# Optimization experiments

Measured on AMD Instinct MI355X. Metric: run time of the kernel, lower is better.

## Reference

```python
import jax, jax.numpy as jnp
import numpy as np

B, N, NB, NORB = 8, 128, 32, 128  # batch, particles, single-body basis size, orbitals


def _offdiag_idx(n):
    # [N, N-1] indices of j != i, matching remove_diag with an aux (feature) axis
    return np.stack([np.concatenate([np.arange(i), np.arange(i + 1, n)]) for i in range(n)])


def setup_inputs() -> dict:
    key = jax.random.key(0)
    k1, k2 = jax.random.split(key)
    chi = jax.random.normal(k1, (B, N, NB), dtype=jnp.float32)
    # param('backflow_coeff', normal(stddev=0.01), (Nb*Nb, n_orbitals))
    backflow_coeff = 0.01 * jax.random.normal(k2, (NB * NB, NORB), dtype=jnp.float32)
    return {"chi": chi, "backflow_coeff": backflow_coeff}


def reference(chi, backflow_coeff):
    b, n, nb = chi.shape
    # basis_combine_backflow: chi_munu_ij[b,i,j, k*Nb + l] = chi[b,j,k] * chi[b,i,l]
    # (meshgrid(a=chi_i, b=chi_j) with indexing='xy' -> prod[k,l] = chi_i[l]*chi_j[k], raveled)
    pair = jnp.einsum('bjk,bil->bijkl', chi, chi).reshape(b, n, n, nb * nb)
    # remove_diag(..., has_aux_axis=True): drop j == i along axis 2 -> [B, N, N-1, Nb^2]
    idx = jnp.asarray(_offdiag_idx(n))
    pair = pair[:, jnp.arange(n)[:, None], idx, :]
    # mean over neighbors j != i -> [B, N, Nb^2]
    basis = pair.mean(axis=-2)
    # BF = basis @ backflow_coeff -> [B, N, n_orbitals]
    return basis @ backflow_coeff
```

## Files before the change

### kernel.cpp

```cpp
#include <hip/hip_runtime.h>
#include <hip/hip_bf16.h>

#define B_    8
#define N_    128
#define NB_   32
#define NORB_ 128
#define RPB   32
#define OPB   16
#define THREADS 256

using bf16x8 = __attribute__((ext_vector_type(8))) short;
using f32x4  = __attribute__((ext_vector_type(4))) float;

__global__ __launch_bounds__(THREADS) void bobf_kernel(
    const float* __restrict__ chi,
    const float* __restrict__ W,
    float* __restrict__ out)
{
    __shared__ float wt[1024][18];
    __shared__ float Sp[8][NB_];
    __shared__ float S[NB_];
    __shared__ __align__(16) float xr_[RPB][36];
    __shared__ float yr_[RPB][36];
    __shared__ float red2[4][RPB][20];

    const int t   = threadIdx.x;
    const int blk = blockIdx.x;
    const int b    = blk >> 5;
    const int rowg = (blk >> 3) & 3;
    const int og   = blk & 7;
    const int i0   = rowg * RPB;
    const int o0   = og * OPB;

    #pragma unroll
    for (int e = 0; e < 32; ++e) {
        const int c  = e * THREADS + t;
        const int kl = c >> 3, cc = c & 7;
        const float2 v = *(const float2*)(W + kl * NORB_ + o0 + cc * 2);
        *(float2*)&wt[kl][cc * 2] = v;
    }

    {
        const int k = t & 31;
        const int g = t >> 5;
        const float* base = chi + (b * N_) * NB_ + k;
        float s = 0.f;
        #pragma unroll
        for (int jj = 0; jj < 16; ++jj) s += base[(g * 16 + jj) * NB_];
        Sp[g][k] = s;
    }
    #pragma unroll
    for (int e = 0; e < 4; ++e) {
        const int idx = e * THREADS + t;
        const int r = idx >> 5, l = idx & 31;
        xr_[r][l] = chi[(b * N_ + i0 + r) * NB_ + l];
    }
    __syncthreads();
    if (t < NB_) {
        float s = 0.f;
        #pragma unroll
        for (int g = 0; g < 8; ++g) s += Sp[g][t];
        S[t] = s;
    }
    __syncthreads();
    {
        const float inv = 1.0f / (float)(N_ - 1);
        #pragma unroll
        for (int e = 0; e < 4; ++e) {
            const int idx = e * THREADS + t;
            const int r = idx >> 5, q = idx & 31;
            yr_[r][q] = (S[q] - xr_[r][q]) * inv;
        }
    }
    __syncthreads();

    const int wv   = t >> 6;
    const int lane = t & 63;
    const int lr = lane & 15;
    const int lg = lane >> 4;
    const int l0 = lg * 8;

    float xa0[8], xa1[8];
    #pragma unroll
    for (int e = 0; e < 8; ++e) {
        xa0[e] = xr_[lr][l0 + e];
        xa1[e] = xr_[16 + lr][l0 + e];
    }

    f32x4 acc0 = {0.f, 0.f, 0.f, 0.f};
    f32x4 acc1 = {0.f, 0.f, 0.f, 0.f};

    #pragma unroll
    for (int ks = 0; ks < 8; ++ks) {
        const int kstep = wv * 8 + ks;
        bf16x8 bf;
        #pragma unroll
        for (int e = 0; e < 8; ++e) {
            const float w0 = wt[kstep * 32 + l0 + e][lr];
            bf[e] = (short)__bfloat16_as_ushort(__float2bfloat16(w0));
        }
        const float y0 = yr_[lr][kstep];
        const float y1 = yr_[16 + lr][kstep];
        bf16x8 af0, af1;
        #pragma unroll
        for (int e = 0; e < 8; ++e) {
            af0[e] = (short)__bfloat16_as_ushort(__float2bfloat16(y0 * xa0[e]));
            af1[e] = (short)__bfloat16_as_ushort(__float2bfloat16(y1 * xa1[e]));
        }
        acc0 = __builtin_amdgcn_mfma_f32_16x16x32_bf16(af0, bf, acc0, 0, 0, 0);
        acc1 = __builtin_amdgcn_mfma_f32_16x16x32_bf16(af1, bf, acc1, 0, 0, 0);
    }

    #pragma unroll
    for (int reg = 0; reg < 4; ++reg) {
        red2[wv][lg * 4 + reg][lr]      = acc0[reg];
        red2[wv][16 + lg * 4 + reg][lr] = acc1[reg];
    }
    __syncthreads();
    #pragma unroll
    for (int e = 0; e < 2; ++e) {
        const int idx = e * THREADS + t;
        const int r = idx >> 4, o = idx & 15;
        const float v = red2[0][r][o] + red2[1][r][o] + red2[2][r][o] + red2[3][r][o];
        out[(b * N_ + i0 + r) * NORB_ + o0 + o] = v;
    }
}

extern "C" void kernel_launch(void* const* d_in, const int* in_sizes, int n_in,
                              void* d_out, int out_size, void* d_ws, size_t ws_size,
                              hipStream_t stream) {
    const float* chi = (const float*)d_in[0];
    const float* W   = (const float*)d_in[1];
    float* out = (float*)d_out;
    dim3 grid(B_ * (N_ / RPB) * (NORB_ / OPB));
    dim3 block(THREADS);
    hipLaunchKernelGGL(bobf_kernel, grid, block, 0, stream, chi, W, out);
}
```

Baseline: 9.854 us.

## Load W fragments directly into registers and double threads per block

Removes the LDS staging of the weight tile. Each lane now loads its bf16 B-fragment values straight from global memory into registers, issued before the chi reductions so the loads overlap that work. The block grows to 512 threads (8 waves), each wave taking 4 k-steps instead of 8. The final cross-wave reduction now sums 8 partials. The direct global loads are strided (one column per lane), which trades coalescing for skipping the LDS round trip and one sync's worth of staging.

```diff
diff --git a/kernel.cpp b/kernel.cpp
--- a/kernel.cpp
+++ b/kernel.cpp
@@ -7,7 +7,7 @@
 #define NORB_ 128
 #define RPB   32
 #define OPB   16
-#define THREADS 256
+#define THREADS 512
 
 using bf16x8 = __attribute__((ext_vector_type(8))) short;
 using f32x4  = __attribute__((ext_vector_type(4))) float;
@@ -17,12 +17,11 @@
     const float* __restrict__ W,
     float* __restrict__ out)
 {
-    __shared__ float wt[1024][18];
-    __shared__ float Sp[8][NB_];
+    __shared__ float Sp[16][NB_];
     __shared__ float S[NB_];
     __shared__ __align__(16) float xr_[RPB][36];
     __shared__ float yr_[RPB][36];
-    __shared__ float red2[4][RPB][20];
+    __shared__ float red2[8][RPB][20];
 
     const int t   = threadIdx.x;
     const int blk = blockIdx.x;
@@ -32,12 +31,20 @@
     const int i0   = rowg * RPB;
     const int o0   = og * OPB;
 
+    const int wv   = t >> 6;
+    const int lane = t & 63;
+    const int lr = lane & 15;
+    const int lg = lane >> 4;
+    const int l0 = lg * 8;
+
+    float wf[4][8];
     #pragma unroll
-    for (int e = 0; e < 32; ++e) {
-        const int c  = e * THREADS + t;
-        const int kl = c >> 3, cc = c & 7;
-        const float2 v = *(const float2*)(W + kl * NORB_ + o0 + cc * 2);
-        *(float2*)&wt[kl][cc * 2] = v;
+    for (int ks = 0; ks < 4; ++ks) {
+        const int kstep = wv * 4 + ks;
+        const float* wp = W + (kstep * 32 + l0) * NORB_ + o0 + lr;
+        #pragma unroll
+        for (int e = 0; e < 8; ++e)
+            wf[ks][e] = wp[e * NORB_];
     }
 
     {
@@ -46,11 +53,11 @@
         const float* base = chi + (b * N_) * NB_ + k;
         float s = 0.f;
         #pragma unroll
-        for (int jj = 0; jj < 16; ++jj) s += base[(g * 16 + jj) * NB_];
+        for (int jj = 0; jj < 8; ++jj) s += base[(g * 8 + jj) * NB_];
         Sp[g][k] = s;
     }
     #pragma unroll
-    for (int e = 0; e < 4; ++e) {
+    for (int e = 0; e < 2; ++e) {
         const int idx = e * THREADS + t;
         const int r = idx >> 5, l = idx & 31;
         xr_[r][l] = chi[(b * N_ + i0 + r) * NB_ + l];
@@ -59,14 +66,14 @@
     if (t < NB_) {
         float s = 0.f;
         #pragma unroll
-        for (int g = 0; g < 8; ++g) s += Sp[g][t];
+        for (int g = 0; g < 16; ++g) s += Sp[g][t];
         S[t] = s;
     }
     __syncthreads();
     {
         const float inv = 1.0f / (float)(N_ - 1);
         #pragma unroll
-        for (int e = 0; e < 4; ++e) {
+        for (int e = 0; e < 2; ++e) {
             const int idx = e * THREADS + t;
             const int r = idx >> 5, q = idx & 31;
             yr_[r][q] = (S[q] - xr_[r][q]) * inv;
@@ -74,11 +81,12 @@
     }
     __syncthreads();
 
-    const int wv   = t >> 6;
-    const int lane = t & 63;
-    const int lr = lane & 15;
-    const int lg = lane >> 4;
-    const int l0 = lg * 8;
+    bf16x8 bfr[4];
+    #pragma unroll
+    for (int ks = 0; ks < 4; ++ks)
+        #pragma unroll
+        for (int e = 0; e < 8; ++e)
+            bfr[ks][e] = (short)__bfloat16_as_ushort(__float2bfloat16(wf[ks][e]));
 
     float xa0[8], xa1[8];
     #pragma unroll
@@ -87,28 +95,25 @@
         xa1[e] = xr_[16 + lr][l0 + e];
     }
 
+    bf16x8 af0[4], af1[4];
+    #pragma unroll
+    for (int ks = 0; ks < 4; ++ks) {
+        const int kstep = wv * 4 + ks;
+        const float y0 = yr_[lr][kstep];
+        const float y1 = yr_[16 + lr][kstep];
+        #pragma unroll
+        for (int e = 0; e < 8; ++e) {
+            af0[ks][e] = (short)__bfloat16_as_ushort(__float2bfloat16(y0 * xa0[e]));
+            af1[ks][e] = (short)__bfloat16_as_ushort(__float2bfloat16(y1 * xa1[e]));
+        }
+    }
+
     f32x4 acc0 = {0.f, 0.f, 0.f, 0.f};
     f32x4 acc1 = {0.f, 0.f, 0.f, 0.f};
-
     #pragma unroll
-    for (int ks = 0; ks < 8; ++ks) {
-        const int kstep = wv * 8 + ks;
-        bf16x8 bf;
-        #pragma unroll
-        for (int e = 0; e < 8; ++e) {
-            const float w0 = wt[kstep * 32 + l0 + e][lr];
-            bf[e] = (short)__bfloat16_as_ushort(__float2bfloat16(w0));
-        }
-        const float y0 = yr_[lr][kstep];
-        const float y1 = yr_[16 + lr][kstep];
-        bf16x8 af0, af1;
-        #pragma unroll
-        for (int e = 0; e < 8; ++e) {
-            af0[e] = (short)__bfloat16_as_ushort(__float2bfloat16(y0 * xa0[e]));
-            af1[e] = (short)__bfloat16_as_ushort(__float2bfloat16(y1 * xa1[e]));
-        }
-        acc0 = __builtin_amdgcn_mfma_f32_16x16x32_bf16(af0, bf, acc0, 0, 0, 0);
-        acc1 = __builtin_amdgcn_mfma_f32_16x16x32_bf16(af1, bf, acc1, 0, 0, 0);
+    for (int ks = 0; ks < 4; ++ks) {
+        acc0 = __builtin_amdgcn_mfma_f32_16x16x32_bf16(af0[ks], bfr[ks], acc0, 0, 0, 0);
+        acc1 = __builtin_amdgcn_mfma_f32_16x16x32_bf16(af1[ks], bfr[ks], acc1, 0, 0, 0);
     }
 
     #pragma unroll
@@ -117,11 +122,11 @@
         red2[wv][16 + lg * 4 + reg][lr] = acc1[reg];
     }
     __syncthreads();
-    #pragma unroll
-    for (int e = 0; e < 2; ++e) {
-        const int idx = e * THREADS + t;
-        const int r = idx >> 4, o = idx & 15;
-        const float v = red2[0][r][o] + red2[1][r][o] + red2[2][r][o] + red2[3][r][o];
+    {
+        const int r = t >> 4, o = t & 15;
+        float v = 0.f;
+        #pragma unroll
+        for (int w8 = 0; w8 < 8; ++w8) v += red2[w8][r][o];
         out[(b * N_ + i0 + r) * NORB_ + o0 + o] = v;
     }
 }
```

Result: no change. 9.673 us (-1.8%).
